# Kernel tuning notes

Hardware: AMD Instinct MI355X
Metric: run time of the kernel (lower is better)

Reference implementation:

```python
import jax, jax.numpy as jnp
import numpy as np

N_EMBD = 1024
N_HEAD = 16
HEAD_DIM = N_EMBD // N_HEAD
EPS = 1e-8


def rmsnorm(x, scale):
    return x * jax.lax.rsqrt(jnp.mean(x * x, axis=-1, keepdims=True) + EPS) * scale


def setup_inputs() -> dict:
    key = jax.random.key(0)
    ks = jax.random.split(key, 7)
    B, L, D = 4, 2048, N_EMBD
    s = lambda fan_in: 1.0 / np.sqrt(fan_in)
    return {
        "x": jax.random.normal(ks[0], (B, L, D), jnp.float32),
        "norm1_scale": jnp.ones((D,), jnp.float32),
        "w_qkv": jax.random.normal(ks[1], (D, 3 * D), jnp.float32) * s(D),
        "w_proj": jax.random.normal(ks[2], (D, D), jnp.float32) * s(D),
        "norm2_scale": jnp.ones((D,), jnp.float32),
        "w_fc1": jax.random.normal(ks[3], (D, 4 * D), jnp.float32) * s(D),
        "w_fc2": jax.random.normal(ks[4], (4 * D, D), jnp.float32) * s(4 * D),
    }


def reference(x, norm1_scale, w_qkv, w_proj, norm2_scale, w_fc1, w_fc2):
    B, L, D = x.shape
    H, hd = N_HEAD, HEAD_DIM

    # --- attention sub-block ---
    h = rmsnorm(x, norm1_scale)
    qkv = h @ w_qkv  # [B, L, 3D]
    q, k, v = jnp.split(qkv, 3, axis=-1)
    q = q.reshape(B, L, H, hd).transpose(0, 2, 1, 3)  # [B, H, L, hd]
    k = k.reshape(B, L, H, hd).transpose(0, 2, 1, 3)
    v = v.reshape(B, L, H, hd).transpose(0, 2, 1, 3)
    att = jnp.einsum("bhqd,bhkd->bhqk", q, k) * (hd ** -0.5)
    att = jax.nn.softmax(att, axis=-1)  # bidirectional, no mask
    out = jnp.einsum("bhqk,bhkd->bhqd", att, v)
    out = out.transpose(0, 2, 1, 3).reshape(B, L, D)
    x = x + out @ w_proj

    # --- MLP sub-block ---
    h = rmsnorm(x, norm2_scale)
    x = x + jax.nn.gelu(h @ w_fc1, approximate=False) @ w_fc2
    return x
```

## Files before the change

### kernel.cpp

```cpp
#include <hip/hip_runtime.h>
#include <hip/hip_bf16.h>
#include <cmath>


typedef __bf16 bf16x8 __attribute__((ext_vector_type(8)));
typedef __bf16 bf16x2 __attribute__((ext_vector_type(2)));
typedef float f32x4 __attribute__((ext_vector_type(4)));

__device__ __forceinline__ float bf2f(unsigned short u) {
  union { unsigned int i; float f; } c; c.i = ((unsigned int)u) << 16; return c.f;
}
__device__ __forceinline__ unsigned short f2bf(float f) {
  union { unsigned int i; float f; } c; c.f = f;
  unsigned int r = c.i + 0x7fffu + ((c.i >> 16) & 1u);
  return (unsigned short)(r >> 16);
}

__device__ __forceinline__ bool probe_bf16(const void* p) {
  return *reinterpret_cast<const unsigned int*>(p) == 0x3F803F80u;
}
__device__ __forceinline__ float ldext(const void* p, size_t i, bool isbf) {
  return isbf ? bf2f(reinterpret_cast<const unsigned short*>(p)[i])
              : reinterpret_cast<const float*>(p)[i];
}

__device__ __forceinline__ void cp16(const unsigned short* g, unsigned short* l) {
  __builtin_amdgcn_global_load_lds(
      (const __attribute__((address_space(1))) unsigned int*)g,
      (__attribute__((address_space(3))) unsigned int*)l,
      16, 0, 0);
}

template <int CTRL>
__device__ __forceinline__ float dpp_ror(float x) {
  union { int i; float f; } a, r;
  a.f = x;
  r.i = __builtin_amdgcn_update_dpp(0, a.i, CTRL, 0xF, 0xF, false);
  return r.f;
}
__device__ __forceinline__ float rowsum16(float x) {
  x += dpp_ror<0x121>(x);
  x += dpp_ror<0x122>(x);
  x += dpp_ror<0x124>(x);
  x += dpp_ror<0x128>(x);
  return x;
}

__global__ __launch_bounds__(256) void transpose_any(
    const void* __restrict__ in, unsigned short* __restrict__ out,
    int R, int C, const void* __restrict__ probe) {
  const bool isbf = probe_bf16(probe);
  __shared__ unsigned short tile[32][33];
  const int bx = blockIdx.x * 32;
  const int by = blockIdx.y * 32;
  const int tx = threadIdx.x & 31, ty = threadIdx.x >> 5;
#pragma unroll
  for (int i = 0; i < 32; i += 8)
    tile[ty + i][tx] = f2bf(ldext(in, (size_t)(by + ty + i) * C + bx + tx, isbf));
  __syncthreads();
#pragma unroll
  for (int i = 0; i < 32; i += 8)
    out[(size_t)(bx + ty + i) * R + by + tx] = tile[tx][ty + i];
}

__device__ __forceinline__ void rmsnorm_body(
    const float v0, const float v1, const float v2, const float v3,
    const void* scale, bool isbf, unsigned short* outrow, int tid) {
  float ss = v0 * v0 + v1 * v1 + v2 * v2 + v3 * v3;
#pragma unroll
  for (int m = 32; m >= 1; m >>= 1) ss += __shfl_xor(ss, m);
  __shared__ float red[4];
  if ((tid & 63) == 0) red[tid >> 6] = ss;
  __syncthreads();
  ss = red[0] + red[1] + red[2] + red[3];
  const float rstd = rsqrtf(ss * (1.0f / 1024.0f) + 1e-8f);
  ushort4 o;
  o.x = f2bf(v0 * rstd * ldext(scale, tid * 4 + 0, isbf));
  o.y = f2bf(v1 * rstd * ldext(scale, tid * 4 + 1, isbf));
  o.z = f2bf(v2 * rstd * ldext(scale, tid * 4 + 2, isbf));
  o.w = f2bf(v3 * rstd * ldext(scale, tid * 4 + 3, isbf));
  reinterpret_cast<ushort4*>(outrow)[tid] = o;
}

__global__ __launch_bounds__(256) void rmsnorm_ext(
    const void* __restrict__ x, const void* __restrict__ scale,
    unsigned short* __restrict__ out, const void* __restrict__ probe) {
  const bool isbf = probe_bf16(probe);
  const int row = blockIdx.x, tid = threadIdx.x;
  float v0, v1, v2, v3;
  if (isbf) {
    ushort4 u = reinterpret_cast<const ushort4*>(x)[(size_t)row * 256 + tid];
    v0 = bf2f(u.x); v1 = bf2f(u.y); v2 = bf2f(u.z); v3 = bf2f(u.w);
  } else {
    float4 f = reinterpret_cast<const float4*>(x)[(size_t)row * 256 + tid];
    v0 = f.x; v1 = f.y; v2 = f.z; v3 = f.w;
  }
  rmsnorm_body(v0, v1, v2, v3, scale, isbf, out + (size_t)row * 1024, tid);
}

__global__ __launch_bounds__(256) void rmsnorm_int(
    const unsigned short* __restrict__ x, const void* __restrict__ scale,
    unsigned short* __restrict__ out, const void* __restrict__ probe) {
  const bool isbf = probe_bf16(probe);
  const int row = blockIdx.x, tid = threadIdx.x;
  ushort4 u = reinterpret_cast<const ushort4*>(x + (size_t)row * 1024)[tid];
  rmsnorm_body(bf2f(u.x), bf2f(u.y), bf2f(u.z), bf2f(u.w),
               scale, isbf, out + (size_t)row * 1024, tid);
}

template <int EPI, typename OutT>
__global__ __launch_bounds__(256) void gemm_bt(
    const unsigned short* __restrict__ A, const unsigned short* __restrict__ BT,
    OutT* __restrict__ C, const void* __restrict__ Res,
    int M, int N, int K, const void* __restrict__ probe) {
  __shared__ __align__(16) unsigned short As[128 * 64];
  __shared__ __align__(16) unsigned short Bs[128 * 64];
  const int tid = threadIdx.x;
  const int lane = tid & 63;
  const int w = tid >> 6;
  const int quad = lane >> 4;
  const int l16 = lane & 15;
  const int wr = w >> 1, wc = w & 1;
  const int m0 = blockIdx.y * 128;
  const int n0 = blockIdx.x * 128;

  const f32x4 zero = {0.f, 0.f, 0.f, 0.f};
  f32x4 acc[4][4];
#pragma unroll
  for (int i = 0; i < 4; ++i)
#pragma unroll
    for (int j = 0; j < 4; ++j) acc[i][j] = zero;

  for (int kt = 0; kt < K; kt += 64) {
#pragma unroll
    for (int i = 0; i < 4; ++i) {
      const int cb = (i * 4 + w) * 64;
      const int c = cb + lane;
      const int row = c >> 3;
      const int gc = (c & 7) ^ (row & 7);
      cp16(A + (size_t)(m0 + row) * K + kt + gc * 8, As + (size_t)cb * 8);
      cp16(BT + (size_t)(n0 + row) * K + kt + gc * 8, Bs + (size_t)cb * 8);
    }
    __syncthreads();

#pragma unroll
    for (int kk = 0; kk < 2; ++kk) {
      bf16x8 af[4], bfr[4];
#pragma unroll
      for (int mi = 0; mi < 4; ++mi)
        af[mi] = *reinterpret_cast<const bf16x8*>(
            As + (wr * 64 + mi * 16 + l16) * 64 + ((((kk << 2) + quad) ^ (l16 & 7)) << 3));
#pragma unroll
      for (int ni = 0; ni < 4; ++ni)
        bfr[ni] = *reinterpret_cast<const bf16x8*>(
            Bs + (wc * 64 + ni * 16 + l16) * 64 + ((((kk << 2) + quad) ^ (l16 & 7)) << 3));
#pragma unroll
      for (int mi = 0; mi < 4; ++mi)
#pragma unroll
        for (int ni = 0; ni < 4; ++ni)
          acc[mi][ni] = __builtin_amdgcn_mfma_f32_16x16x32_bf16(af[mi], bfr[ni], acc[mi][ni], 0, 0, 0);
    }
    __syncthreads();
  }

  const bool pb = (EPI == 3) ? probe_bf16(probe) : true;
#pragma unroll
  for (int mi = 0; mi < 4; ++mi) {
#pragma unroll
    for (int reg = 0; reg < 4; ++reg) {
      const int row = m0 + wr * 64 + mi * 16 + quad * 4 + reg;
#pragma unroll
      for (int ni = 0; ni < 4; ++ni) {
        const int col = n0 + wc * 64 + ni * 16 + l16;
        float v = acc[mi][ni][reg];
        if (EPI == 1) v = 0.5f * v * (1.0f + erff(v * 0.70710678118654752f));
        if (EPI == 2) v += bf2f(reinterpret_cast<const unsigned short*>(Res)[(size_t)row * N + col]);
        if (EPI == 3) v += ldext(Res, (size_t)row * N + col, pb);
        if (EPI == 4 && col < 1024) v *= 0.18033688011112042f;
        if constexpr (sizeof(OutT) == 2)
          C[(size_t)row * N + col] = f2bf(v);
        else
          C[(size_t)row * N + col] = v;
      }
    }
  }
}

__global__ __launch_bounds__(256) void flash_attn(
    const unsigned short* __restrict__ qkv, unsigned short* __restrict__ out) {
  __shared__ __align__(16) unsigned short Ks[2][64 * 64];
  __shared__ __align__(16) unsigned short Vt[64 * 64];
  __shared__ __align__(16) unsigned short Ps[128 * 64];
  const int L = 2048, DQ = 3072, D = 1024;
  const int qt = blockIdx.x, h = blockIdx.y, b = blockIdx.z;
  const int tid = threadIdx.x, lane = tid & 63, w = tid >> 6;
  const int quad = lane >> 4, l16 = lane & 15;
  const int woff = w * 32;
  const unsigned short* base = qkv + (size_t)b * L * DQ;

  int4 vreg[2];
#pragma unroll
  for (int i = 0; i < 2; ++i) {
    int c = i * 256 + tid;
    int key = c >> 3, d8 = (c & 7) << 3;
    vreg[i] = *reinterpret_cast<const int4*>(base + (size_t)key * DQ + 2048 + h * 64 + d8);
  }
#pragma unroll
  for (int i = 0; i < 2; ++i) {
    const int S = (i * 4 + w) * 64;
    const int key = (S >> 3) + (lane >> 3);
    const int ch = (lane & 7) ^ (lane >> 3);
    cp16(base + (size_t)key * DQ + 1024 + h * 64 + ch * 8, &Ks[0][S * 8]);
  }

#pragma unroll
  for (int i = 0; i < 4; ++i) {
    int c = i * 256 + tid;
    int r = c >> 3, d8 = (c & 7) << 3;
    *reinterpret_cast<int4*>(Ps + r * 64 + d8) =
        *reinterpret_cast<const int4*>(base + (size_t)(qt * 128 + r) * DQ + h * 64 + d8);
  }
  __syncthreads();
  bf16x8 qf[2][2];
#pragma unroll
  for (int mi = 0; mi < 2; ++mi)
#pragma unroll
    for (int kc = 0; kc < 2; ++kc)
      qf[mi][kc] = *reinterpret_cast<const bf16x8*>(Ps + (woff + mi * 16 + l16) * 64 + kc * 32 + quad * 8);

  const f32x4 zero = {0.f, 0.f, 0.f, 0.f};
  f32x4 l_v[2];
  f32x4 o[2][4];
#pragma unroll
  for (int mi = 0; mi < 2; ++mi) {
    l_v[mi] = zero;
#pragma unroll
    for (int nd = 0; nd < 4; ++nd) o[mi][nd] = zero;
  }

  for (int kt = 0; kt < L; kt += 64) {
    const int cur = (kt >> 6) & 1;
    __syncthreads();

#pragma unroll
    for (int i = 0; i < 2; ++i) {
      int c = i * 256 + tid;
      int key = c >> 3, d8 = (c & 7) << 3;
      unsigned short vb[8];
      *reinterpret_cast<int4*>(vb) = vreg[i];
#pragma unroll
      for (int j = 0; j < 8; ++j)
        Vt[(d8 + j) * 64 + (key ^ d8 ^ ((j & 4) << 3))] = vb[j];
    }

    {
      int ktn = kt + 64; if (ktn >= L) ktn = 0;
      const unsigned short* kb = base + (size_t)ktn * DQ;
#pragma unroll
      for (int i = 0; i < 2; ++i) {
        const int S = (i * 4 + w) * 64;
        const int key = (S >> 3) + (lane >> 3);
        const int ch = (lane & 7) ^ (lane >> 3);
        cp16(kb + (size_t)key * DQ + 1024 + h * 64 + ch * 8, &Ks[cur ^ 1][S * 8]);
      }
#pragma unroll
      for (int i = 0; i < 2; ++i) {
        int c = i * 256 + tid;
        int key = c >> 3, d8 = (c & 7) << 3;
        vreg[i] = *reinterpret_cast<const int4*>(kb + (size_t)key * DQ + 2048 + h * 64 + d8);
      }
    }

    f32x4 s[2][4];
#pragma unroll
    for (int mi = 0; mi < 2; ++mi)
#pragma unroll
      for (int ni = 0; ni < 4; ++ni) s[mi][ni] = zero;
#pragma unroll
    for (int kc = 0; kc < 2; ++kc) {
      bf16x8 kf[4];
#pragma unroll
      for (int ni = 0; ni < 4; ++ni)
        kf[ni] = *reinterpret_cast<const bf16x8*>(
            &Ks[cur][(ni * 16 + l16) * 64 + ((((kc << 2) + quad) ^ (l16 & 7)) << 3)]);
#pragma unroll
      for (int mi = 0; mi < 2; ++mi)
#pragma unroll
        for (int ni = 0; ni < 4; ++ni)
          s[mi][ni] = __builtin_amdgcn_mfma_f32_16x16x32_bf16(qf[mi][kc], kf[ni], s[mi][ni], 0, 0, 0);
    }

#pragma unroll
    for (int mi = 0; mi < 2; ++mi) {
      f32x4 acc = zero;
#pragma unroll
      for (int ni = 0; ni < 4; ++ni) {
        f32x4 p;
#pragma unroll
        for (int r = 0; r < 4; ++r) p[r] = __builtin_amdgcn_exp2f(s[mi][ni][r]);
        s[mi][ni] = p;
        acc += p;
      }
      l_v[mi] += acc;
    }

#pragma unroll
    for (int mi = 0; mi < 2; ++mi)
#pragma unroll
      for (int ni = 0; ni < 4; ni += 2)
#pragma unroll
        for (int reg = 0; reg < 4; ++reg) {
          union { bf16x2 v; unsigned int u; } pk;
          pk.v[0] = (__bf16)s[mi][ni][reg];
          pk.v[1] = (__bf16)s[mi][ni + 1][reg];
          const int row = (woff + mi * 16 + quad * 4 + reg) * 64;
          Ps[row + ((ni * 16 + l16) ^ (quad << 4))] = (unsigned short)pk.u;
          Ps[row + (((ni + 1) * 16 + l16) ^ (quad << 4))] = (unsigned short)(pk.u >> 16);
        }
    __syncthreads();

#pragma unroll
    for (int kc = 0; kc < 2; ++kc) {
      bf16x8 pf[2], vf[4];
#pragma unroll
      for (int mi = 0; mi < 2; ++mi)
        pf[mi] = *reinterpret_cast<const bf16x8*>(
            &Ps[(woff + mi * 16 + l16) * 64 + ((kc * 32 + quad * 8) ^ ((l16 >> 2) << 4))]);
#pragma unroll
      for (int nd = 0; nd < 4; ++nd) {
        const int d = nd * 16 + l16;
        vf[nd] = *reinterpret_cast<const bf16x8*>(
            &Vt[d * 64 + ((kc * 32 + quad * 8) ^ (d & 56) ^ ((l16 & 4) << 3))]);
      }
#pragma unroll
      for (int mi = 0; mi < 2; ++mi)
#pragma unroll
        for (int nd = 0; nd < 4; ++nd)
          o[mi][nd] = __builtin_amdgcn_mfma_f32_16x16x32_bf16(pf[mi], vf[nd], o[mi][nd], 0, 0, 0);
    }
  }

#pragma unroll
  for (int mi = 0; mi < 2; ++mi) {
#pragma unroll
    for (int reg = 0; reg < 4; ++reg) {
      const float lsum = rowsum16(l_v[mi][reg]);
      const float inv = 1.0f / lsum;
      const int row = qt * 128 + woff + mi * 16 + quad * 4 + reg;
#pragma unroll
      for (int nd = 0; nd < 4; ++nd) {
        const int col = h * 64 + nd * 16 + l16;
        out[(size_t)(b * L + row) * D + col] = f2bf(o[mi][nd][reg] * inv);
      }
    }
  }
}

extern "C" void kernel_launch(void* const* d_in, const int* in_sizes, int n_in,
                              void* d_out, int out_size, void* d_ws, size_t ws_size,
                              hipStream_t stream) {
  const void* x      = d_in[0];
  const void* n1s    = d_in[1];
  const void* w_qkv  = d_in[2];
  const void* w_proj = d_in[3];
  const void* n2s    = d_in[4];
  const void* w_fc1  = d_in[5];
  const void* w_fc2  = d_in[6];
  float* out = (float*)d_out;
  char* ws = (char*)d_ws;

  const int M = 8192;
  unsigned short* wqkvT  = (unsigned short*)(ws + ((size_t)0   << 20));
  unsigned short* wprojT = (unsigned short*)(ws + ((size_t)6   << 20));
  unsigned short* wfc1T  = (unsigned short*)(ws + ((size_t)8   << 20));
  unsigned short* wfc2T  = (unsigned short*)(ws + ((size_t)16  << 20));
  unsigned short* h      = (unsigned short*)(ws + ((size_t)24  << 20));
  unsigned short* qkvb   = (unsigned short*)(ws + ((size_t)40  << 20));
  unsigned short* attn   = (unsigned short*)(ws + ((size_t)88  << 20));
  unsigned short* x2     = (unsigned short*)(ws + ((size_t)104 << 20));
  unsigned short* g      = qkvb;

  transpose_any<<<dim3(96, 32), 256, 0, stream>>>(w_qkv, wqkvT, 1024, 3072, n1s);
  transpose_any<<<dim3(32, 32), 256, 0, stream>>>(w_proj, wprojT, 1024, 1024, n1s);
  transpose_any<<<dim3(128, 32), 256, 0, stream>>>(w_fc1, wfc1T, 1024, 4096, n1s);
  transpose_any<<<dim3(32, 128), 256, 0, stream>>>(w_fc2, wfc2T, 4096, 1024, n1s);

  rmsnorm_ext<<<M, 256, 0, stream>>>(x, n1s, h, n1s);
  gemm_bt<4, unsigned short><<<dim3(24, 64), 256, 0, stream>>>(h, wqkvT, qkvb, nullptr, M, 3072, 1024, n1s);
  flash_attn<<<dim3(16, 16, 4), 256, 0, stream>>>(qkvb, attn);
  gemm_bt<3, unsigned short><<<dim3(8, 64), 256, 0, stream>>>(attn, wprojT, x2, x, M, 1024, 1024, n1s);
  rmsnorm_int<<<M, 256, 0, stream>>>(x2, n2s, h, n1s);
  gemm_bt<1, unsigned short><<<dim3(32, 64), 256, 0, stream>>>(h, wfc1T, g, nullptr, M, 4096, 1024, n1s);
  gemm_bt<2, float><<<dim3(8, 64), 256, 0, stream>>>(g, wfc2T, out, x2, M, 1024, 4096, n1s);
}
```

Before: 599.6 us.

## Write V transposed from QKV GEMM epilogue and rework flash attention pipeline

The QKV GEMM gets a new epilogue that writes the V block into a separate buffer in transposed [b, d, key] layout. Flash attention can then load V tiles straight into LDS with async copies, double-buffered like K, instead of scattering V through registers into LDS each iteration. It also computes S transposed (K as the A operand), so the exp'd probabilities stay in registers as the A-fragment for P·V. This removes the Ps LDS round trip and one barrier per tile, and adds explicit waitcnt, barrier and setprio scheduling. The cost is an extra transposed V write in the GEMM epilogue and reuse of the x2 buffer as scratch.

```diff
diff --git a/kernel.cpp b/kernel.cpp
--- a/kernel.cpp
+++ b/kernel.cpp
@@ -29,21 +29,6 @@
       (const __attribute__((address_space(1))) unsigned int*)g,
       (__attribute__((address_space(3))) unsigned int*)l,
       16, 0, 0);
-}
-
-template <int CTRL>
-__device__ __forceinline__ float dpp_ror(float x) {
-  union { int i; float f; } a, r;
-  a.f = x;
-  r.i = __builtin_amdgcn_update_dpp(0, a.i, CTRL, 0xF, 0xF, false);
-  return r.f;
-}
-__device__ __forceinline__ float rowsum16(float x) {
-  x += dpp_ror<0x121>(x);
-  x += dpp_ror<0x122>(x);
-  x += dpp_ror<0x124>(x);
-  x += dpp_ror<0x128>(x);
-  return x;
 }
 
 __global__ __launch_bounds__(256) void transpose_any(
@@ -163,6 +148,28 @@
     __syncthreads();
   }
 
+  if constexpr (EPI == 5) {
+    if (n0 >= 2048) {
+      unsigned short* vt = (unsigned short*)Res;
+#pragma unroll
+      for (int mi = 0; mi < 4; ++mi) {
+        const int r0 = m0 + wr * 64 + mi * 16 + quad * 4;
+        const int bq = r0 >> 11;
+        const int key = r0 & 2047;
+#pragma unroll
+        for (int ni = 0; ni < 4; ++ni) {
+          const int vcol = n0 - 2048 + wc * 64 + ni * 16 + l16;
+          ushort4 o4;
+          o4.x = f2bf(acc[mi][ni][0]); o4.y = f2bf(acc[mi][ni][1]);
+          o4.z = f2bf(acc[mi][ni][2]); o4.w = f2bf(acc[mi][ni][3]);
+          *reinterpret_cast<ushort4*>(
+              vt + (((size_t)(bq * 1024 + vcol)) << 11) + key) = o4;
+        }
+      }
+      return;
+    }
+  }
+
   const bool pb = (EPI == 3) ? probe_bf16(probe) : true;
 #pragma unroll
   for (int mi = 0; mi < 4; ++mi) {
@@ -176,7 +183,7 @@
         if (EPI == 1) v = 0.5f * v * (1.0f + erff(v * 0.70710678118654752f));
         if (EPI == 2) v += bf2f(reinterpret_cast<const unsigned short*>(Res)[(size_t)row * N + col]);
         if (EPI == 3) v += ldext(Res, (size_t)row * N + col, pb);
-        if (EPI == 4 && col < 1024) v *= 0.18033688011112042f;
+        if ((EPI == 4 || EPI == 5) && col < 1024) v *= 0.18033688011112042f;
         if constexpr (sizeof(OutT) == 2)
           C[(size_t)row * N + col] = f2bf(v);
         else
@@ -187,170 +194,158 @@
 }
 
 __global__ __launch_bounds__(256) void flash_attn(
-    const unsigned short* __restrict__ qkv, unsigned short* __restrict__ out) {
+    const unsigned short* __restrict__ qkv,
+    const unsigned short* __restrict__ vT,
+    unsigned short* __restrict__ out) {
   __shared__ __align__(16) unsigned short Ks[2][64 * 64];
-  __shared__ __align__(16) unsigned short Vt[64 * 64];
-  __shared__ __align__(16) unsigned short Ps[128 * 64];
+  __shared__ __align__(16) unsigned short Vs[2][64 * 64];
   const int L = 2048, DQ = 3072, D = 1024;
   const int qt = blockIdx.x, h = blockIdx.y, b = blockIdx.z;
   const int tid = threadIdx.x, lane = tid & 63, w = tid >> 6;
   const int quad = lane >> 4, l16 = lane & 15;
   const int woff = w * 32;
   const unsigned short* base = qkv + (size_t)b * L * DQ;
-
-  int4 vreg[2];
-#pragma unroll
-  for (int i = 0; i < 2; ++i) {
-    int c = i * 256 + tid;
-    int key = c >> 3, d8 = (c & 7) << 3;
-    vreg[i] = *reinterpret_cast<const int4*>(base + (size_t)key * DQ + 2048 + h * 64 + d8);
-  }
-#pragma unroll
-  for (int i = 0; i < 2; ++i) {
-    const int S = (i * 4 + w) * 64;
-    const int key = (S >> 3) + (lane >> 3);
-    const int ch = (lane & 7) ^ (lane >> 3);
-    cp16(base + (size_t)key * DQ + 1024 + h * 64 + ch * 8, &Ks[0][S * 8]);
-  }
-
+  const unsigned short* vbase = vT + (size_t)(b * 1024 + h * 64) * 2048;
+
+  unsigned short* Qs = &Vs[0][0];
 #pragma unroll
   for (int i = 0; i < 4; ++i) {
-    int c = i * 256 + tid;
-    int r = c >> 3, d8 = (c & 7) << 3;
-    *reinterpret_cast<int4*>(Ps + r * 64 + d8) =
-        *reinterpret_cast<const int4*>(base + (size_t)(qt * 128 + r) * DQ + h * 64 + d8);
-  }
-  __syncthreads();
+    const int cb = i * 256 + w * 64;
+    const int c = cb + lane;
+    const int r = c >> 3, d8 = (c & 7) << 3;
+    cp16(base + (size_t)(qt * 128 + r) * DQ + h * 64 + d8, Qs + ((size_t)cb << 3));
+  }
+  asm volatile("s_waitcnt vmcnt(0)" ::: "memory");
+  __builtin_amdgcn_s_barrier();
+  __builtin_amdgcn_sched_barrier(0);
   bf16x8 qf[2][2];
 #pragma unroll
-  for (int mi = 0; mi < 2; ++mi)
+  for (int mj = 0; mj < 2; ++mj)
 #pragma unroll
     for (int kc = 0; kc < 2; ++kc)
-      qf[mi][kc] = *reinterpret_cast<const bf16x8*>(Ps + (woff + mi * 16 + l16) * 64 + kc * 32 + quad * 8);
+      qf[mj][kc] = *reinterpret_cast<const bf16x8*>(
+          Qs + (woff + mj * 16 + l16) * 64 + kc * 32 + quad * 8);
+  asm volatile("s_waitcnt lgkmcnt(0)" ::: "memory");
+  __builtin_amdgcn_sched_barrier(0);
+  __builtin_amdgcn_s_barrier();
+
+  auto STAGE = [&](int s, int kt0) {
+#pragma unroll
+    for (int i = 0; i < 2; ++i) {
+      const int cb = i * 256 + w * 64;
+      const int cd = cb + lane;
+      const int m = cd >> 3, cc = cd & 7;
+      const int gk = ((m >> 4) & 1) * 32 + ((m >> 2) & 3) * 8 + (m >> 5) * 4 + (m & 3);
+      const int gc = cc ^ (m & 7);
+      cp16(base + (size_t)(kt0 + gk) * DQ + 1024 + h * 64 + gc * 8,
+           &Ks[s][(size_t)cb << 3]);
+    }
+#pragma unroll
+    for (int i = 0; i < 2; ++i) {
+      const int cb = i * 256 + w * 64;
+      const int cd = cb + lane;
+      const int d = cd >> 3, cc = cd & 7;
+      const int gc = cc ^ (d & 7);
+      cp16(vbase + (size_t)d * 2048 + kt0 + gc * 8, &Vs[s][(size_t)cb << 3]);
+    }
+  };
+
+  STAGE(0, 0);
 
   const f32x4 zero = {0.f, 0.f, 0.f, 0.f};
-  f32x4 l_v[2];
+  f32x4 l4[2] = {zero, zero};
   f32x4 o[2][4];
 #pragma unroll
-  for (int mi = 0; mi < 2; ++mi) {
-    l_v[mi] = zero;
-#pragma unroll
-    for (int nd = 0; nd < 4; ++nd) o[mi][nd] = zero;
-  }
+  for (int mj = 0; mj < 2; ++mj)
+#pragma unroll
+    for (int nd = 0; nd < 4; ++nd) o[mj][nd] = zero;
 
   for (int kt = 0; kt < L; kt += 64) {
     const int cur = (kt >> 6) & 1;
-    __syncthreads();
-
-#pragma unroll
-    for (int i = 0; i < 2; ++i) {
-      int c = i * 256 + tid;
-      int key = c >> 3, d8 = (c & 7) << 3;
-      unsigned short vb[8];
-      *reinterpret_cast<int4*>(vb) = vreg[i];
-#pragma unroll
-      for (int j = 0; j < 8; ++j)
-        Vt[(d8 + j) * 64 + (key ^ d8 ^ ((j & 4) << 3))] = vb[j];
-    }
-
-    {
-      int ktn = kt + 64; if (ktn >= L) ktn = 0;
-      const unsigned short* kb = base + (size_t)ktn * DQ;
-#pragma unroll
-      for (int i = 0; i < 2; ++i) {
-        const int S = (i * 4 + w) * 64;
-        const int key = (S >> 3) + (lane >> 3);
-        const int ch = (lane & 7) ^ (lane >> 3);
-        cp16(kb + (size_t)key * DQ + 1024 + h * 64 + ch * 8, &Ks[cur ^ 1][S * 8]);
-      }
-#pragma unroll
-      for (int i = 0; i < 2; ++i) {
-        int c = i * 256 + tid;
-        int key = c >> 3, d8 = (c & 7) << 3;
-        vreg[i] = *reinterpret_cast<const int4*>(kb + (size_t)key * DQ + 2048 + h * 64 + d8);
-      }
-    }
-
-    f32x4 s[2][4];
-#pragma unroll
-    for (int mi = 0; mi < 2; ++mi)
-#pragma unroll
-      for (int ni = 0; ni < 4; ++ni) s[mi][ni] = zero;
+    if (kt + 64 < L) {
+      STAGE(cur ^ 1, kt + 64);
+      asm volatile("s_waitcnt vmcnt(4)" ::: "memory");
+    } else {
+      asm volatile("s_waitcnt vmcnt(0)" ::: "memory");
+    }
+    __builtin_amdgcn_s_barrier();
+    __builtin_amdgcn_sched_barrier(0);
+
+    f32x4 sv[4][2];
+#pragma unroll
+    for (int ki = 0; ki < 4; ++ki)
+#pragma unroll
+      for (int mj = 0; mj < 2; ++mj) sv[ki][mj] = zero;
 #pragma unroll
     for (int kc = 0; kc < 2; ++kc) {
       bf16x8 kf[4];
 #pragma unroll
-      for (int ni = 0; ni < 4; ++ni)
-        kf[ni] = *reinterpret_cast<const bf16x8*>(
-            &Ks[cur][(ni * 16 + l16) * 64 + ((((kc << 2) + quad) ^ (l16 & 7)) << 3)]);
-#pragma unroll
-      for (int mi = 0; mi < 2; ++mi)
-#pragma unroll
-        for (int ni = 0; ni < 4; ++ni)
-          s[mi][ni] = __builtin_amdgcn_mfma_f32_16x16x32_bf16(qf[mi][kc], kf[ni], s[mi][ni], 0, 0, 0);
-    }
-
-#pragma unroll
-    for (int mi = 0; mi < 2; ++mi) {
-      f32x4 acc = zero;
-#pragma unroll
-      for (int ni = 0; ni < 4; ++ni) {
-        f32x4 p;
-#pragma unroll
-        for (int r = 0; r < 4; ++r) p[r] = __builtin_amdgcn_exp2f(s[mi][ni][r]);
-        s[mi][ni] = p;
-        acc += p;
+      for (int ki = 0; ki < 4; ++ki)
+        kf[ki] = *reinterpret_cast<const bf16x8*>(
+            &Ks[cur][(ki * 16 + l16) * 64 + ((((kc << 2) + quad) ^ (l16 & 7)) << 3)]);
+      __builtin_amdgcn_s_setprio(1);
+#pragma unroll
+      for (int ki = 0; ki < 4; ++ki)
+#pragma unroll
+        for (int mj = 0; mj < 2; ++mj)
+          sv[ki][mj] = __builtin_amdgcn_mfma_f32_16x16x32_bf16(kf[ki], qf[mj][kc], sv[ki][mj], 0, 0, 0);
+      __builtin_amdgcn_s_setprio(0);
+    }
+
+    bf16x8 pf[2][2];
+#pragma unroll
+    for (int mj = 0; mj < 2; ++mj)
+#pragma unroll
+      for (int kc = 0; kc < 2; ++kc) {
+        f32x4 pa, pb;
+#pragma unroll
+        for (int r = 0; r < 4; ++r) pa[r] = __builtin_amdgcn_exp2f(sv[kc][mj][r]);
+#pragma unroll
+        for (int r = 0; r < 4; ++r) pb[r] = __builtin_amdgcn_exp2f(sv[kc + 2][mj][r]);
+        l4[mj] += pa;
+        l4[mj] += pb;
+        bf16x8 t;
+        t[0] = (__bf16)pa[0]; t[1] = (__bf16)pa[1]; t[2] = (__bf16)pa[2]; t[3] = (__bf16)pa[3];
+        t[4] = (__bf16)pb[0]; t[5] = (__bf16)pb[1]; t[6] = (__bf16)pb[2]; t[7] = (__bf16)pb[3];
+        pf[mj][kc] = t;
       }
-      l_v[mi] += acc;
-    }
-
-#pragma unroll
-    for (int mi = 0; mi < 2; ++mi)
-#pragma unroll
-      for (int ni = 0; ni < 4; ni += 2)
-#pragma unroll
-        for (int reg = 0; reg < 4; ++reg) {
-          union { bf16x2 v; unsigned int u; } pk;
-          pk.v[0] = (__bf16)s[mi][ni][reg];
-          pk.v[1] = (__bf16)s[mi][ni + 1][reg];
-          const int row = (woff + mi * 16 + quad * 4 + reg) * 64;
-          Ps[row + ((ni * 16 + l16) ^ (quad << 4))] = (unsigned short)pk.u;
-          Ps[row + (((ni + 1) * 16 + l16) ^ (quad << 4))] = (unsigned short)(pk.u >> 16);
-        }
-    __syncthreads();
 
 #pragma unroll
     for (int kc = 0; kc < 2; ++kc) {
-      bf16x8 pf[2], vf[4];
-#pragma unroll
-      for (int mi = 0; mi < 2; ++mi)
-        pf[mi] = *reinterpret_cast<const bf16x8*>(
-            &Ps[(woff + mi * 16 + l16) * 64 + ((kc * 32 + quad * 8) ^ ((l16 >> 2) << 4))]);
-#pragma unroll
-      for (int nd = 0; nd < 4; ++nd) {
-        const int d = nd * 16 + l16;
+      bf16x8 vf[4];
+#pragma unroll
+      for (int nd = 0; nd < 4; ++nd)
         vf[nd] = *reinterpret_cast<const bf16x8*>(
-            &Vt[d * 64 + ((kc * 32 + quad * 8) ^ (d & 56) ^ ((l16 & 4) << 3))]);
-      }
-#pragma unroll
-      for (int mi = 0; mi < 2; ++mi)
+            &Vs[cur][(nd * 16 + l16) * 64 + ((((kc << 2) + quad) ^ (l16 & 7)) << 3)]);
+      __builtin_amdgcn_s_setprio(1);
+#pragma unroll
+      for (int mj = 0; mj < 2; ++mj)
 #pragma unroll
         for (int nd = 0; nd < 4; ++nd)
-          o[mi][nd] = __builtin_amdgcn_mfma_f32_16x16x32_bf16(pf[mi], vf[nd], o[mi][nd], 0, 0, 0);
-    }
-  }
-
-#pragma unroll
-  for (int mi = 0; mi < 2; ++mi) {
-#pragma unroll
-    for (int reg = 0; reg < 4; ++reg) {
-      const float lsum = rowsum16(l_v[mi][reg]);
-      const float inv = 1.0f / lsum;
-      const int row = qt * 128 + woff + mi * 16 + quad * 4 + reg;
+          o[mj][nd] = __builtin_amdgcn_mfma_f32_16x16x32_bf16(pf[mj][kc], vf[nd], o[mj][nd], 0, 0, 0);
+      __builtin_amdgcn_s_setprio(0);
+    }
+
+    if (kt + 64 < L) {
+      asm volatile("s_waitcnt lgkmcnt(0)" ::: "memory");
+      __builtin_amdgcn_sched_barrier(0);
+      __builtin_amdgcn_s_barrier();
+    }
+  }
+
+#pragma unroll
+  for (int mj = 0; mj < 2; ++mj) {
+    float lp = l4[mj][0] + l4[mj][1] + l4[mj][2] + l4[mj][3];
+    lp += __shfl_xor(lp, 16);
+    lp += __shfl_xor(lp, 32);
+#pragma unroll
+    for (int r = 0; r < 4; ++r) {
+      const float inv = 1.0f / __shfl(lp, quad * 4 + r);
+      const int row = qt * 128 + woff + mj * 16 + quad * 4 + r;
 #pragma unroll
       for (int nd = 0; nd < 4; ++nd) {
         const int col = h * 64 + nd * 16 + l16;
-        out[(size_t)(b * L + row) * D + col] = f2bf(o[mi][nd][reg] * inv);
+        out[(size_t)(b * L + row) * D + col] = f2bf(o[mj][nd][r] * inv);
       }
     }
   }
@@ -379,6 +374,7 @@
   unsigned short* attn   = (unsigned short*)(ws + ((size_t)88  << 20));
   unsigned short* x2     = (unsigned short*)(ws + ((size_t)104 << 20));
   unsigned short* g      = qkvb;
+  unsigned short* vT     = x2;
 
   transpose_any<<<dim3(96, 32), 256, 0, stream>>>(w_qkv, wqkvT, 1024, 3072, n1s);
   transpose_any<<<dim3(32, 32), 256, 0, stream>>>(w_proj, wprojT, 1024, 1024, n1s);
@@ -386,8 +382,8 @@
   transpose_any<<<dim3(32, 128), 256, 0, stream>>>(w_fc2, wfc2T, 4096, 1024, n1s);
 
   rmsnorm_ext<<<M, 256, 0, stream>>>(x, n1s, h, n1s);
-  gemm_bt<4, unsigned short><<<dim3(24, 64), 256, 0, stream>>>(h, wqkvT, qkvb, nullptr, M, 3072, 1024, n1s);
-  flash_attn<<<dim3(16, 16, 4), 256, 0, stream>>>(qkvb, attn);
+  gemm_bt<5, unsigned short><<<dim3(24, 64), 256, 0, stream>>>(h, wqkvT, qkvb, vT, M, 3072, 1024, n1s);
+  flash_attn<<<dim3(16, 16, 4), 256, 0, stream>>>(qkvb, vT, attn);
   gemm_bt<3, unsigned short><<<dim3(8, 64), 256, 0, stream>>>(attn, wprojT, x2, x, M, 1024, 1024, n1s);
   rmsnorm_int<<<M, 256, 0, stream>>>(x2, n2s, h, n1s);
   gemm_bt<1, unsigned short><<<dim3(32, 64), 256, 0, stream>>>(h, wfc1T, g, nullptr, M, 4096, 1024, n1s);
```

After: 568.9 us. -5.1%, faster.
